# Optimization experiments

Hardware: AMD Instinct MI355X
Metric: run time of the kernel (lower is better)

Reference implementation:

```python
import jax, jax.numpy as jnp
import numpy as np

D_MODEL = 1024
NUM_HEADS = 16
HEAD_DIM = D_MODEL // NUM_HEADS
THETA = 10000.0


def _init_linear(key, d_out, d_in):
    sigma = np.sqrt(2.0 / (d_in + d_out))
    w = jax.random.truncated_normal(key, -3.0, 3.0, (d_out, d_in), dtype=jnp.float32)
    return w * sigma


def setup_inputs() -> dict:
    key = jax.random.key(0)
    kh, kq, kk, kv, ko = jax.random.split(key, 5)
    h = jax.random.normal(kh, (2, 2048, D_MODEL), dtype=jnp.float32)
    return {
        "h": h,
        "wq": _init_linear(kq, D_MODEL, D_MODEL),
        "wk": _init_linear(kk, D_MODEL, D_MODEL),
        "wv": _init_linear(kv, D_MODEL, D_MODEL),
        "wo": _init_linear(ko, D_MODEL, D_MODEL),
    }


def _rope(x, pos):
    # x: [B, H, T, dh]; rotate interleaved pairs (..., 2k, 2k+1)
    dh = x.shape[-1]
    freq = THETA ** (-jnp.arange(0, dh // 2, dtype=jnp.float32) / (dh // 2))
    ang = pos[:, None] * freq[None, :]            # [T, dh/2]
    cos, sin = jnp.cos(ang), jnp.sin(ang)
    xr = x.reshape(*x.shape[:-1], dh // 2, 2)
    x0, x1 = xr[..., 0], xr[..., 1]
    out = jnp.stack((cos * x0 - sin * x1, sin * x0 + cos * x1), axis=-1)
    return out.reshape(x.shape)


def reference(h, wq, wk, wv, wo):
    B, T, D = h.shape
    Hn, dh = NUM_HEADS, HEAD_DIM

    def split_heads(x):  # [B,T,D] -> [B,H,T,dh]
        return x.reshape(B, T, Hn, dh).transpose(0, 2, 1, 3)

    Q = split_heads(h @ wq.T)
    K = split_heads(h @ wk.T)
    V = split_heads(h @ wv.T)

    pos = jnp.arange(T, dtype=jnp.float32)
    Q = _rope(Q, pos)
    K = _rope(K, pos)

    scores = jnp.einsum('bhqd,bhkd->bhqk', Q, K) / jnp.sqrt(jnp.float32(dh))
    mask = jnp.tril(jnp.ones((T, T), dtype=bool))
    scores = jnp.where(mask, scores, -jnp.inf)
    attn = jax.nn.softmax(scores, axis=-1)
    out = jnp.einsum('bhqk,bhkd->bhqd', attn, V)   # [B,H,T,dh]
    out = out.transpose(0, 2, 1, 3).reshape(B, T, D)
    return out @ wo.T
```

## Files before the change

### kernel.cpp

```cpp
#include <hip/hip_runtime.h>
#include <math.h>

typedef __bf16 bf16_t;
typedef __bf16 v8bf __attribute__((ext_vector_type(8)));
typedef __bf16 v4bf __attribute__((ext_vector_type(4)));
typedef float  v4f  __attribute__((ext_vector_type(4)));

#define AS1 __attribute__((address_space(1)))
#define AS3 __attribute__((address_space(3)))

static __device__ __forceinline__ void load_lds16(const bf16_t* g, bf16_t* l) {
    __builtin_amdgcn_global_load_lds((AS1 void*)const_cast<bf16_t*>(g),
                                     (AS3 void*)l, 16, 0, 0);
}

__global__ __launch_bounds__(256) void cvt_fp32_bf16(
    const float* __restrict__ h,  const float* __restrict__ wq,
    const float* __restrict__ wk, const float* __restrict__ wv,
    const float* __restrict__ wo,
    bf16_t* __restrict__ hb,  bf16_t* __restrict__ wqb,
    bf16_t* __restrict__ wkb, bf16_t* __restrict__ wvb,
    bf16_t* __restrict__ wob)
{
    const size_t HM = (size_t)4 << 20;
    const size_t i8 = ((size_t)blockIdx.x * 256 + threadIdx.x) * 8;
    const float* src; bf16_t* dst; size_t off;
    if (i8 < HM) { src = h; dst = hb; off = i8; }
    else {
        const size_t r = (i8 - HM) >> 20;
        off = (i8 - HM) & (((size_t)1 << 20) - 1);
        src = (r == 0) ? wq  : (r == 1) ? wk  : (r == 2) ? wv  : wo;
        dst = (r == 0) ? wqb : (r == 1) ? wkb : (r == 2) ? wvb : wob;
    }
    const float4 a = *(const float4*)(src + off);
    const float4 b = *(const float4*)(src + off + 4);
    v8bf o;
    o[0]=(bf16_t)a.x; o[1]=(bf16_t)a.y; o[2]=(bf16_t)a.z; o[3]=(bf16_t)a.w;
    o[4]=(bf16_t)b.x; o[5]=(bf16_t)b.y; o[6]=(bf16_t)b.z; o[7]=(bf16_t)b.w;
    *(v8bf*)(dst + off) = o;
}

static __device__ __forceinline__ void fast_sincos(float ang, float* sn, float* cs) {
    float rv = ang * 0.15915494309189535f;
    rv -= floorf(rv);
    const float a = rv * 6.283185307179586f;
    *sn = __sinf(a);
    *cs = __cosf(a);
}

__global__ __launch_bounds__(256) void qkv_gemm_rope(
    const bf16_t* __restrict__ A,
    const bf16_t* __restrict__ wq,
    const bf16_t* __restrict__ wk,
    const bf16_t* __restrict__ wv,
    bf16_t* __restrict__ qo, bf16_t* __restrict__ ko, bf16_t* __restrict__ vo)
{
    __shared__ __align__(16) bf16_t smem[17408];
    bf16_t* As = smem;
    bf16_t* Bs = smem + 4096;

    const int tid = threadIdx.x;
    const int n0  = blockIdx.x * 128;
    const int m0  = blockIdx.y * 128;
    const int sel = n0 >> 10;
    const bf16_t* W = (sel == 0) ? wq : (sel == 1) ? wk : wv;
    const int wr0 = n0 & 1023;

    const int wave = tid >> 6;
    const int lane = tid & 63;
    const int l16  = lane & 15;
    const int quad = lane >> 4;
    const int wrow = (wave >> 1) * 64;
    const int wcol = (wave & 1) * 64;

    v4f acc[4][4];
    #pragma unroll
    for (int i = 0; i < 4; ++i)
        #pragma unroll
        for (int j = 0; j < 4; ++j) acc[i][j] = (v4f)(0.0f);

    for (int kt = 0; kt < 32; ++kt) {
        const int k0 = kt * 32;
        #pragma unroll
        for (int rep = 0; rep < 2; ++rep) {
            const int c   = rep * 256 + tid;
            const int row = c >> 2;
            const int col = (c & 3) * 8;
            load_lds16(A + (size_t)(m0 + row) * 1024 + k0 + col, &As[c * 8]);
            load_lds16(W + (size_t)(wr0 + row) * 1024 + k0 + col, &Bs[c * 8]);
        }
        __syncthreads();

        v8bf af[4], bfb[4];
        #pragma unroll
        for (int i = 0; i < 4; ++i) {
            af[i]  = *(const v8bf*)&As[(wrow + i * 16 + l16) * 32 + quad * 8];
            bfb[i] = *(const v8bf*)&Bs[(wcol + i * 16 + l16) * 32 + quad * 8];
        }
        #pragma unroll
        for (int i = 0; i < 4; ++i)
            #pragma unroll
            for (int j = 0; j < 4; ++j)
                acc[i][j] = __builtin_amdgcn_mfma_f32_16x16x32_bf16(
                    af[i], bfb[j], acc[i][j], 0, 0, 0);
        __syncthreads();
    }

    bf16_t* Ls = smem + wave * 4352;
    const int bq     = (m0 + wrow) >> 11;
    const int hd     = ((n0 + wcol) >> 6) & 15;
    const int t_base = (m0 + wrow) & 2047;

    if (sel < 2) {
        bf16_t* OUT = (sel == 0) ? qo : ko;
        #pragma unroll
        for (int i = 0; i < 4; ++i) {
            #pragma unroll
            for (int j = 0; j < 4; ++j) {
                #pragma unroll
                for (int r = 0; r < 4; ++r) {
                    const int mrow = i * 16 + quad * 4 + r;
                    const int dcol = j * 16 + l16;
                    float v = acc[i][j][r];
                    const float vp = __shfl_xor(v, 1);
                    const int t  = t_base + mrow;
                    const int kk = dcol >> 1;
                    const float freq = exp2f((float)kk * -0.4152410118609203f);
                    float sn, cs;
                    fast_sincos((float)t * freq, &sn, &cs);
                    v = ((dcol & 1) == 0) ? (cs * v - sn * vp) : (sn * vp + cs * v);
                    Ls[mrow * 68 + dcol] = (bf16_t)v;
                }
            }
        }
        #pragma unroll
        for (int s = 0; s < 8; ++s) {
            const int row = s * 8 + (lane >> 3);
            const int off = (lane & 7) * 8;
            const v8bf vv = *(const v8bf*)&Ls[row * 68 + off];
            *(v8bf*)(OUT + (((size_t)(bq * 16 + hd) * 2048) + t_base + row) * 64 + off) = vv;
        }
    } else {
        #pragma unroll
        for (int i = 0; i < 4; ++i)
            #pragma unroll
            for (int j = 0; j < 4; ++j) {
                v4bf p;
                #pragma unroll
                for (int r = 0; r < 4; ++r) p[r] = (bf16_t)acc[i][j][r];
                *(v4bf*)&Ls[(j * 16 + l16) * 68 + i * 16 + quad * 4] = p;
            }
        #pragma unroll
        for (int s = 0; s < 8; ++s) {
            const int drow = s * 8 + (lane >> 3);
            const int off  = (lane & 7) * 8;
            const v8bf vv = *(const v8bf*)&Ls[drow * 68 + off];
            *(v8bf*)(vo + (((size_t)(bq * 16 + hd) * 64) + drow) * 2048 + t_base + off) = vv;
        }
    }
}

__global__ __launch_bounds__(256) void attn_mfma(
    const bf16_t* __restrict__ qg,
    const bf16_t* __restrict__ kg,
    const bf16_t* __restrict__ vtg,
    bf16_t* __restrict__ og)
{
    __shared__ __align__(16) bf16_t Ks[64 * 72];
    __shared__ __align__(16) bf16_t Vs[64 * 72];
    __shared__ __align__(16) bf16_t Ps[4][16 * 72];

    const int tid  = threadIdx.x;
    const int wave = tid >> 6;
    const int lane = tid & 63;
    const int l16  = lane & 15;
    const int quad = lane >> 4;
    const int bx   = blockIdx.x;
    const int bh   = blockIdx.y;
    const int b = bh >> 4, hh = bh & 15;

    #pragma unroll
    for (int pass = 0; pass < 2; ++pass) {
        const int qt = pass ? bx : (31 - bx);

        const bf16_t* qrow = qg + (((size_t)bh * 2048) + (size_t)qt * 64 + wave * 16 + l16) * 64;
        v8bf qf[2];
        qf[0] = *(const v8bf*)(qrow + quad * 8);
        qf[1] = *(const v8bf*)(qrow + 32 + quad * 8);
        #pragma unroll
        for (int e = 0; e < 8; ++e) {
            qf[0][e] = (bf16_t)((float)qf[0][e] * 0.125f);
            qf[1][e] = (bf16_t)((float)qf[1][e] * 0.125f);
        }

        float m_r[4], l_r[4];
        v4f o_acc[4];
        #pragma unroll
        for (int r = 0; r < 4; ++r) { m_r[r] = -1e30f; l_r[r] = 0.0f; }
        #pragma unroll
        for (int dblk = 0; dblk < 4; ++dblk) o_acc[dblk] = (v4f)(0.0f);

        v8bf kreg[2], vreg[2];
        #pragma unroll
        for (int rep = 0; rep < 2; ++rep) {
            const int c = rep * 256 + tid;
            const int row = c >> 3, col = (c & 7) * 8;
            kreg[rep] = *(const v8bf*)(kg + (((size_t)bh * 2048) + row) * 64 + col);
            vreg[rep] = *(const v8bf*)(vtg + ((size_t)bh * 64 + row) * 2048 + col);
        }

        for (int kt = 0; kt <= qt; ++kt) {
            __syncthreads();
            #pragma unroll
            for (int rep = 0; rep < 2; ++rep) {
                const int c = rep * 256 + tid;
                const int row = c >> 3, col = (c & 7) * 8;
                *(v8bf*)&Ks[row * 72 + col] = kreg[rep];
                *(v8bf*)&Vs[row * 72 + col] = vreg[rep];
            }
            __syncthreads();

            if (kt < qt) {
                #pragma unroll
                for (int rep = 0; rep < 2; ++rep) {
                    const int c = rep * 256 + tid;
                    const int row = c >> 3, col = (c & 7) * 8;
                    kreg[rep] = *(const v8bf*)(kg + (((size_t)bh * 2048) + (size_t)(kt + 1) * 64 + row) * 64 + col);
                    vreg[rep] = *(const v8bf*)(vtg + ((size_t)bh * 64 + row) * 2048 + (size_t)(kt + 1) * 64 + col);
                }
            }

            v4f s_acc[4];
            #pragma unroll
            for (int kblk = 0; kblk < 4; ++kblk) s_acc[kblk] = (v4f)(0.0f);
            #pragma unroll
            for (int kblk = 0; kblk < 4; ++kblk)
                #pragma unroll
                for (int dblk = 0; dblk < 2; ++dblk) {
                    const v8bf kf = *(const v8bf*)&Ks[(kblk * 16 + l16) * 72 + dblk * 32 + quad * 8];
                    s_acc[kblk] = __builtin_amdgcn_mfma_f32_16x16x32_bf16(
                        qf[dblk], kf, s_acc[kblk], 0, 0, 0);
                }

            if (kt == qt) {
                #pragma unroll
                for (int kblk = 0; kblk < 4; ++kblk)
                    #pragma unroll
                    for (int r = 0; r < 4; ++r)
                        if (kblk * 16 + l16 > wave * 16 + quad * 4 + r)
                            s_acc[kblk][r] = -1e30f;
            }

            float alpha[4];
            #pragma unroll
            for (int r = 0; r < 4; ++r) {
                float mx = fmaxf(fmaxf(s_acc[0][r], s_acc[1][r]),
                                 fmaxf(s_acc[2][r], s_acc[3][r]));
                #pragma unroll
                for (int msk = 1; msk < 16; msk <<= 1) mx = fmaxf(mx, __shfl_xor(mx, msk));
                const float m_new = fmaxf(m_r[r], mx);
                float s = 0.0f;
                #pragma unroll
                for (int kblk = 0; kblk < 4; ++kblk) {
                    const float p = __expf(s_acc[kblk][r] - m_new);
                    s_acc[kblk][r] = p;
                    s += p;
                }
                #pragma unroll
                for (int msk = 1; msk < 16; msk <<= 1) s += __shfl_xor(s, msk);
                alpha[r] = __expf(m_r[r] - m_new);
                l_r[r] = l_r[r] * alpha[r] + s;
                m_r[r] = m_new;
            }

            #pragma unroll
            for (int kblk = 0; kblk < 4; ++kblk)
                #pragma unroll
                for (int r = 0; r < 4; ++r)
                    Ps[wave][(quad * 4 + r) * 72 + kblk * 16 + l16] = (bf16_t)s_acc[kblk][r];
            #pragma unroll
            for (int dblk = 0; dblk < 4; ++dblk)
                #pragma unroll
                for (int r = 0; r < 4; ++r)
                    o_acc[dblk][r] *= alpha[r];

            v8bf pf[2];
            pf[0] = *(const v8bf*)&Ps[wave][l16 * 72 + quad * 8];
            pf[1] = *(const v8bf*)&Ps[wave][l16 * 72 + 32 + quad * 8];
            #pragma unroll
            for (int dblk = 0; dblk < 4; ++dblk)
                #pragma unroll
                for (int kk = 0; kk < 2; ++kk) {
                    const v8bf vf = *(const v8bf*)&Vs[(dblk * 16 + l16) * 72 + kk * 32 + quad * 8];
                    o_acc[dblk] = __builtin_amdgcn_mfma_f32_16x16x32_bf16(
                        pf[kk], vf, o_acc[dblk], 0, 0, 0);
                }
        }

        #pragma unroll
        for (int r = 0; r < 4; ++r) {
            const float inv_l = 1.0f / l_r[r];
            const size_t t    = (size_t)qt * 64 + wave * 16 + quad * 4 + r;
            const size_t base = ((size_t)b * 2048 + t) * 1024 + hh * 64;
            #pragma unroll
            for (int dblk = 0; dblk < 4; ++dblk)
                og[base + dblk * 16 + l16] = (bf16_t)(o_acc[dblk][r] * inv_l);
        }
        __syncthreads();
    }
}

__global__ __launch_bounds__(256) void out_gemm(
    const bf16_t* __restrict__ A,
    const bf16_t* __restrict__ W,
    float* __restrict__ C)
{
    __shared__ __align__(16) float smemf[8448];
    bf16_t* As = (bf16_t*)smemf;
    bf16_t* Bs = As + 4096;

    const int tid = threadIdx.x;
    const int n0  = blockIdx.x * 128;
    const int m0  = blockIdx.y * 128;

    const int wave = tid >> 6;
    const int lane = tid & 63;
    const int l16  = lane & 15;
    const int quad = lane >> 4;
    const int wrow = (wave >> 1) * 64;
    const int wcol = (wave & 1) * 64;

    v4f acc[4][4];
    #pragma unroll
    for (int i = 0; i < 4; ++i)
        #pragma unroll
        for (int j = 0; j < 4; ++j) acc[i][j] = (v4f)(0.0f);

    for (int kt = 0; kt < 32; ++kt) {
        const int k0 = kt * 32;
        #pragma unroll
        for (int rep = 0; rep < 2; ++rep) {
            const int c   = rep * 256 + tid;
            const int row = c >> 2;
            const int col = (c & 3) * 8;
            load_lds16(A + (size_t)(m0 + row) * 1024 + k0 + col, &As[c * 8]);
            load_lds16(W + (size_t)(n0 + row) * 1024 + k0 + col, &Bs[c * 8]);
        }
        __syncthreads();

        v8bf af[4], bfb[4];
        #pragma unroll
        for (int i = 0; i < 4; ++i) {
            af[i]  = *(const v8bf*)&As[(wrow + i * 16 + l16) * 32 + quad * 8];
            bfb[i] = *(const v8bf*)&Bs[(wcol + i * 16 + l16) * 32 + quad * 8];
        }
        #pragma unroll
        for (int i = 0; i < 4; ++i)
            #pragma unroll
            for (int j = 0; j < 4; ++j)
                acc[i][j] = __builtin_amdgcn_mfma_f32_16x16x32_bf16(
                    af[i], bfb[j], acc[i][j], 0, 0, 0);
        __syncthreads();
    }

    float* Lw = smemf + wave * 2112;
    #pragma unroll
    for (int half = 0; half < 2; ++half) {
        #pragma unroll
        for (int ii = 0; ii < 2; ++ii) {
            const int i = half * 2 + ii;
            #pragma unroll
            for (int j = 0; j < 4; ++j)
                #pragma unroll
                for (int r = 0; r < 4; ++r)
                    Lw[(ii * 16 + quad * 4 + r) * 66 + j * 16 + l16] = acc[i][j][r];
        }
        __syncthreads();
        #pragma unroll
        for (int s = 0; s < 16; ++s) {
            const int row = s * 2 + (lane >> 5);
            const int off = (lane & 31) * 2;
            const float2 vv = *(const float2*)&Lw[row * 66 + off];
            *(float2*)(C + (size_t)(m0 + wrow + half * 32 + row) * 1024 + n0 + wcol + off) = vv;
        }
        __syncthreads();
    }
}

extern "C" void kernel_launch(void* const* d_in, const int* in_sizes, int n_in,
                              void* d_out, int out_size, void* d_ws, size_t ws_size,
                              hipStream_t stream) {
    const float* h  = (const float*)d_in[0];
    const float* wq = (const float*)d_in[1];
    const float* wk = (const float*)d_in[2];
    const float* wv = (const float*)d_in[3];
    const float* wo = (const float*)d_in[4];

    const size_t NH = (size_t)4096 * 1024;
    const size_t NW = (size_t)1024 * 1024;

    bf16_t* hb  = (bf16_t*)d_ws;
    bf16_t* wqb = hb  + NH;
    bf16_t* wkb = wqb + NW;
    bf16_t* wvb = wkb + NW;
    bf16_t* wob = wvb + NW;
    bf16_t* qw  = wob + NW;
    bf16_t* kw  = qw + NH;
    bf16_t* vw  = kw + NH;
    bf16_t* og  = hb;

    cvt_fp32_bf16<<<dim3(4096), dim3(256), 0, stream>>>(
        h, wq, wk, wv, wo, hb, wqb, wkb, wvb, wob);
    qkv_gemm_rope<<<dim3(24, 32), dim3(256), 0, stream>>>(hb, wqb, wkb, wvb, qw, kw, vw);
    attn_mfma<<<dim3(16, 32), dim3(256), 0, stream>>>(qw, kw, vw, og);
    out_gemm<<<dim3(8, 32), dim3(256), 0, stream>>>(og, wob, (float*)d_out);
}
```

Measured before the change: 213.6 us.

## Restructure attention into single-wave blocks reading K/V directly from global

Each attention block now holds one 64-lane wave that handles 16 query rows, giving 2048 blocks paired so causal work stays balanced and bh is interleaved across blocks. The shared-memory K/V staging and its barriers are gone. K and V fragments are loaded straight from global memory into MFMA operands. The MFMA operands are swapped so that score rows lie along lanes, which lets the softmax reductions use two cross-lane shuffles instead of four, and outputs are written as vector stores. This cuts synchronisation and shared-memory traffic, at the cost of K/V global/L2 reads that are no longer shared across waves in a block.

Result: slower. 264.2 us (+23.7%).

```diff
diff --git a/kernel.cpp b/kernel.cpp
--- a/kernel.cpp
+++ b/kernel.cpp
@@ -160,30 +160,34 @@
     }
 }
 
-__global__ __launch_bounds__(256) void attn_mfma(
+__global__ __launch_bounds__(64) void attn_mfma(
     const bf16_t* __restrict__ qg,
     const bf16_t* __restrict__ kg,
     const bf16_t* __restrict__ vtg,
     bf16_t* __restrict__ og)
 {
-    __shared__ __align__(16) bf16_t Ks[64 * 72];
-    __shared__ __align__(16) bf16_t Vs[64 * 72];
-    __shared__ __align__(16) bf16_t Ps[4][16 * 72];
-
-    const int tid  = threadIdx.x;
-    const int wave = tid >> 6;
-    const int lane = tid & 63;
+    __shared__ __align__(16) bf16_t Ps[16 * 72];
+
+    const int lane = threadIdx.x;
     const int l16  = lane & 15;
     const int quad = lane >> 4;
-    const int bx   = blockIdx.x;
-    const int bh   = blockIdx.y;
-    const int b = bh >> 4, hh = bh & 15;
+
+    const int b0 = blockIdx.x;
+    const int s  = b0 >> 3;
+    const int bh = (b0 & 7) * 4 + (s >> 6);
+    const int jp = s & 63;
+    const int b  = bh >> 4, hh = bh & 15;
+
+    const bf16_t* Kb = kg  + (size_t)bh * 2048 * 64;
+    const bf16_t* Vb = vtg + (size_t)bh * 64 * 2048;
 
     #pragma unroll
     for (int pass = 0; pass < 2; ++pass) {
-        const int qt = pass ? bx : (31 - bx);
-
-        const bf16_t* qrow = qg + (((size_t)bh * 2048) + (size_t)qt * 64 + wave * 16 + l16) * 64;
+        const int q16  = pass ? jp : (127 - jp);
+        const int kmax = q16 >> 2;
+        const int qglb = q16 * 16 + l16;
+
+        const bf16_t* qrow = qg + (((size_t)bh * 2048) + qglb) * 64;
         v8bf qf[2];
         qf[0] = *(const v8bf*)(qrow + quad * 8);
         qf[1] = *(const v8bf*)(qrow + 32 + quad * 8);
@@ -193,120 +197,91 @@
             qf[1][e] = (bf16_t)((float)qf[1][e] * 0.125f);
         }
 
-        float m_r[4], l_r[4];
+        float m_r = -1e30f, l_r = 0.0f;
         v4f o_acc[4];
         #pragma unroll
-        for (int r = 0; r < 4; ++r) { m_r[r] = -1e30f; l_r[r] = 0.0f; }
-        #pragma unroll
-        for (int dblk = 0; dblk < 4; ++dblk) o_acc[dblk] = (v4f)(0.0f);
-
-        v8bf kreg[2], vreg[2];
-        #pragma unroll
-        for (int rep = 0; rep < 2; ++rep) {
-            const int c = rep * 256 + tid;
-            const int row = c >> 3, col = (c & 7) * 8;
-            kreg[rep] = *(const v8bf*)(kg + (((size_t)bh * 2048) + row) * 64 + col);
-            vreg[rep] = *(const v8bf*)(vtg + ((size_t)bh * 64 + row) * 2048 + col);
-        }
-
-        for (int kt = 0; kt <= qt; ++kt) {
-            __syncthreads();
-            #pragma unroll
-            for (int rep = 0; rep < 2; ++rep) {
-                const int c = rep * 256 + tid;
-                const int row = c >> 3, col = (c & 7) * 8;
-                *(v8bf*)&Ks[row * 72 + col] = kreg[rep];
-                *(v8bf*)&Vs[row * 72 + col] = vreg[rep];
-            }
-            __syncthreads();
-
-            if (kt < qt) {
-                #pragma unroll
-                for (int rep = 0; rep < 2; ++rep) {
-                    const int c = rep * 256 + tid;
-                    const int row = c >> 3, col = (c & 7) * 8;
-                    kreg[rep] = *(const v8bf*)(kg + (((size_t)bh * 2048) + (size_t)(kt + 1) * 64 + row) * 64 + col);
-                    vreg[rep] = *(const v8bf*)(vtg + ((size_t)bh * 64 + row) * 2048 + (size_t)(kt + 1) * 64 + col);
-                }
-            }
-
+        for (int d = 0; d < 4; ++d) o_acc[d] = (v4f)(0.0f);
+
+        for (int kt = 0; kt <= kmax; ++kt) {
             v4f s_acc[4];
             #pragma unroll
             for (int kblk = 0; kblk < 4; ++kblk) s_acc[kblk] = (v4f)(0.0f);
             #pragma unroll
-            for (int kblk = 0; kblk < 4; ++kblk)
-                #pragma unroll
-                for (int dblk = 0; dblk < 2; ++dblk) {
-                    const v8bf kf = *(const v8bf*)&Ks[(kblk * 16 + l16) * 72 + dblk * 32 + quad * 8];
-                    s_acc[kblk] = __builtin_amdgcn_mfma_f32_16x16x32_bf16(
-                        qf[dblk], kf, s_acc[kblk], 0, 0, 0);
-                }
-
-            if (kt == qt) {
+            for (int kblk = 0; kblk < 4; ++kblk) {
+                const bf16_t* krow = Kb + ((size_t)kt * 64 + kblk * 16 + l16) * 64;
+                const v8bf kf0 = *(const v8bf*)(krow + quad * 8);
+                const v8bf kf1 = *(const v8bf*)(krow + 32 + quad * 8);
+                s_acc[kblk] = __builtin_amdgcn_mfma_f32_16x16x32_bf16(
+                    kf0, qf[0], s_acc[kblk], 0, 0, 0);
+                s_acc[kblk] = __builtin_amdgcn_mfma_f32_16x16x32_bf16(
+                    kf1, qf[1], s_acc[kblk], 0, 0, 0);
+            }
+
+            if (kt == kmax) {
                 #pragma unroll
                 for (int kblk = 0; kblk < 4; ++kblk)
                     #pragma unroll
                     for (int r = 0; r < 4; ++r)
-                        if (kblk * 16 + l16 > wave * 16 + quad * 4 + r)
+                        if (kt * 64 + kblk * 16 + quad * 4 + r > qglb)
                             s_acc[kblk][r] = -1e30f;
             }
 
-            float alpha[4];
-            #pragma unroll
-            for (int r = 0; r < 4; ++r) {
-                float mx = fmaxf(fmaxf(s_acc[0][r], s_acc[1][r]),
-                                 fmaxf(s_acc[2][r], s_acc[3][r]));
-                #pragma unroll
-                for (int msk = 1; msk < 16; msk <<= 1) mx = fmaxf(mx, __shfl_xor(mx, msk));
-                const float m_new = fmaxf(m_r[r], mx);
-                float s = 0.0f;
-                #pragma unroll
-                for (int kblk = 0; kblk < 4; ++kblk) {
+            float mx = -1e30f;
+            #pragma unroll
+            for (int kblk = 0; kblk < 4; ++kblk)
+                #pragma unroll
+                for (int r = 0; r < 4; ++r) mx = fmaxf(mx, s_acc[kblk][r]);
+            mx = fmaxf(mx, __shfl_xor(mx, 16));
+            mx = fmaxf(mx, __shfl_xor(mx, 32));
+            const float m_new = fmaxf(m_r, mx);
+            float ssum = 0.0f;
+            #pragma unroll
+            for (int kblk = 0; kblk < 4; ++kblk)
+                #pragma unroll
+                for (int r = 0; r < 4; ++r) {
                     const float p = __expf(s_acc[kblk][r] - m_new);
                     s_acc[kblk][r] = p;
-                    s += p;
+                    ssum += p;
                 }
-                #pragma unroll
-                for (int msk = 1; msk < 16; msk <<= 1) s += __shfl_xor(s, msk);
-                alpha[r] = __expf(m_r[r] - m_new);
-                l_r[r] = l_r[r] * alpha[r] + s;
-                m_r[r] = m_new;
-            }
-
-            #pragma unroll
-            for (int kblk = 0; kblk < 4; ++kblk)
-                #pragma unroll
-                for (int r = 0; r < 4; ++r)
-                    Ps[wave][(quad * 4 + r) * 72 + kblk * 16 + l16] = (bf16_t)s_acc[kblk][r];
-            #pragma unroll
-            for (int dblk = 0; dblk < 4; ++dblk)
-                #pragma unroll
-                for (int r = 0; r < 4; ++r)
-                    o_acc[dblk][r] *= alpha[r];
-
-            v8bf pf[2];
-            pf[0] = *(const v8bf*)&Ps[wave][l16 * 72 + quad * 8];
-            pf[1] = *(const v8bf*)&Ps[wave][l16 * 72 + 32 + quad * 8];
-            #pragma unroll
-            for (int dblk = 0; dblk < 4; ++dblk)
-                #pragma unroll
-                for (int kk = 0; kk < 2; ++kk) {
-                    const v8bf vf = *(const v8bf*)&Vs[(dblk * 16 + l16) * 72 + kk * 32 + quad * 8];
-                    o_acc[dblk] = __builtin_amdgcn_mfma_f32_16x16x32_bf16(
-                        pf[kk], vf, o_acc[dblk], 0, 0, 0);
-                }
-        }
-
-        #pragma unroll
-        for (int r = 0; r < 4; ++r) {
-            const float inv_l = 1.0f / l_r[r];
-            const size_t t    = (size_t)qt * 64 + wave * 16 + quad * 4 + r;
-            const size_t base = ((size_t)b * 2048 + t) * 1024 + hh * 64;
-            #pragma unroll
-            for (int dblk = 0; dblk < 4; ++dblk)
-                og[base + dblk * 16 + l16] = (bf16_t)(o_acc[dblk][r] * inv_l);
-        }
-        __syncthreads();
+            ssum += __shfl_xor(ssum, 16);
+            ssum += __shfl_xor(ssum, 32);
+            const float alpha = __expf(m_r - m_new);
+            l_r = l_r * alpha + ssum;
+            m_r = m_new;
+
+            #pragma unroll
+            for (int kblk = 0; kblk < 4; ++kblk) {
+                v4bf p;
+                #pragma unroll
+                for (int r = 0; r < 4; ++r) p[r] = (bf16_t)s_acc[kblk][r];
+                *(v4bf*)&Ps[l16 * 72 + kblk * 16 + quad * 4] = p;
+            }
+            #pragma unroll
+            for (int d = 0; d < 4; ++d) o_acc[d] *= alpha;
+
+            v8bf pf0 = *(const v8bf*)&Ps[l16 * 72 + quad * 8];
+            v8bf pf1 = *(const v8bf*)&Ps[l16 * 72 + 32 + quad * 8];
+            #pragma unroll
+            for (int dblk = 0; dblk < 4; ++dblk) {
+                const bf16_t* vrow = Vb + ((size_t)(dblk * 16 + l16)) * 2048 + kt * 64;
+                const v8bf vf0 = *(const v8bf*)(vrow + quad * 8);
+                const v8bf vf1 = *(const v8bf*)(vrow + 32 + quad * 8);
+                o_acc[dblk] = __builtin_amdgcn_mfma_f32_16x16x32_bf16(
+                    vf0, pf0, o_acc[dblk], 0, 0, 0);
+                o_acc[dblk] = __builtin_amdgcn_mfma_f32_16x16x32_bf16(
+                    vf1, pf1, o_acc[dblk], 0, 0, 0);
+            }
+        }
+
+        const float inv_l = 1.0f / l_r;
+        const size_t base = ((size_t)b * 2048 + qglb) * 1024 + hh * 64;
+        #pragma unroll
+        for (int dblk = 0; dblk < 4; ++dblk) {
+            v4bf o;
+            #pragma unroll
+            for (int r = 0; r < 4; ++r) o[r] = (bf16_t)(o_acc[dblk][r] * inv_l);
+            *(v4bf*)(og + base + dblk * 16 + quad * 4) = o;
+        }
     }
 }
 
@@ -412,6 +387,6 @@
     cvt_fp32_bf16<<<dim3(4096), dim3(256), 0, stream>>>(
         h, wq, wk, wv, wo, hb, wqb, wkb, wvb, wob);
     qkv_gemm_rope<<<dim3(24, 32), dim3(256), 0, stream>>>(hb, wqb, wkb, wvb, qw, kw, vw);
-    attn_mfma<<<dim3(16, 32), dim3(256), 0, stream>>>(qw, kw, vw, og);
+    attn_mfma<<<dim3(2048), dim3(64), 0, stream>>>(qw, kw, vw, og);
     out_gemm<<<dim3(8, 32), dim3(256), 0, stream>>>(og, wob, (float*)d_out);
 }
```
